# Kernel tuning notes

Hardware: AMD Instinct MI355X
Metric: run time of the kernel (lower is better)

Reference implementation:

```python
import jax, jax.numpy as jnp
import numpy as np

N = 100000   # nodes
G = 256      # graphs
E = 120000   # edges per relation
IN = 162
HID = 128
R = 5
L = 2        # extra RGCN layers beyond the initial one


def setup_inputs() -> dict:
    key = jax.random.key(0)
    ks = jax.random.split(key, 24)
    s = 0.05
    inp = {
        "X": jax.random.normal(ks[0], (N, IN), jnp.float32),
        "batch": jnp.sort(jax.random.randint(ks[6], (N,), 0, G)),
    }
    for i in range(R):
        inp[f"edge_index{i+1}"] = jax.random.randint(ks[1 + i], (2, E), 0, N)
    # RGCN initial layer params
    inp["W0"] = jax.random.normal(ks[7], (R, IN, HID), jnp.float32) * s
    inp["root0"] = jax.random.normal(ks[8], (IN, HID), jnp.float32) * s
    inp["b0"] = jnp.zeros((HID,), jnp.float32)
    # stacked params for the L hidden RGCN layers
    inp["Wl"] = jax.random.normal(ks[9], (L, R, HID, HID), jnp.float32) * s
    inp["rootl"] = jax.random.normal(ks[10], (L, HID, HID), jnp.float32) * s
    inp["bl"] = jnp.zeros((L, HID), jnp.float32)
    # classification head
    inp["Wc1"] = jax.random.normal(ks[11], (HID, HID), jnp.float32) * s
    inp["bc1"] = jnp.zeros((HID,), jnp.float32)
    inp["Wc2"] = jax.random.normal(ks[12], (HID, HID), jnp.float32) * s
    inp["bc2"] = jnp.zeros((HID,), jnp.float32)
    inp["Wc3"] = jax.random.normal(ks[13], (HID, 1), jnp.float32) * s
    inp["bc3"] = jnp.zeros((1,), jnp.float32)
    return inp


def _seg_mean(msg, dst, num):
    # scatter-mean over destination nodes (PyG RGCNConv uses aggr='mean' per relation)
    s = jax.ops.segment_sum(msg, dst, num_segments=num)
    c = jax.ops.segment_sum(jnp.ones(msg.shape[0], msg.dtype), dst, num_segments=num)
    return s / jnp.maximum(c, 1.0)[:, None]


def _rgcn(x, W, root, b, src, dst):
    # src, dst: [R, E]; W: [R, d_in, d_out]
    msgs = jnp.einsum("ref,rfh->reh", x[src], W)          # [R, E, HID]
    agg = jax.vmap(_seg_mean, in_axes=(0, 0, None))(msgs, dst, N)  # [R, N, HID]
    return x @ root + b + agg.sum(0)


def reference(X, edge_index1, edge_index2, edge_index3, edge_index4, edge_index5,
              batch, W0, root0, b0, Wl, rootl, bl, Wc1, bc1, Wc2, bc2, Wc3, bc3):
    ei = jnp.stack([edge_index1, edge_index2, edge_index3, edge_index4, edge_index5])  # [R,2,E]
    src, dst = ei[:, 0, :], ei[:, 1, :]
    h = jax.nn.relu(_rgcn(X, W0, root0, b0, src, dst))
    for l in range(L):
        h = jax.nn.relu(_rgcn(h, Wl[l], rootl[l], bl[l], src, dst))
    # mean readout over graphs
    s = jax.ops.segment_sum(h, batch, num_segments=G)
    c = jax.ops.segment_sum(jnp.ones((N,), h.dtype), batch, num_segments=G)
    read = s / jnp.maximum(c, 1.0)[:, None]
    h = jax.nn.relu(read @ Wc1 + bc1)
    h = jax.nn.relu(h @ Wc2 + bc2)
    return h @ Wc3 + bc3
```

## Files before the change

### kernel.cpp

```cpp
#include <hip/hip_runtime.h>

#define N_NODES 100000
#define NPAD    100096
#define NTILES  782
#define TPX     98
#define G_GRAPHS 256
#define IN_F 162
#define KPAD0 192
#define HID 128
#define R_REL 5
#define L_LAYERS 2
#define M5 (R_REL * N_NODES)

typedef __attribute__((ext_vector_type(8))) short bf16x8;
typedef __attribute__((ext_vector_type(4))) float f32x4;

__device__ __forceinline__ short f2bf(float f) {
    union { float f; unsigned u; } v; v.f = f;
    unsigned r = (v.u + 0x7fffu + ((v.u >> 16) & 1u)) >> 16;
    return (short)r;
}
__device__ __forceinline__ float bf2f(unsigned short u) {
    union { unsigned u; float f; } v; v.u = ((unsigned)u) << 16;
    return v.f;
}

__global__ void k_count(const int* e0, const int* e1, const int* e2,
                        const int* e3, const int* e4, int* cnt, int E) {
    int gid = blockIdx.x * 256 + threadIdx.x;
    if (gid >= R_REL * E) return;
    int r = gid / E, e = gid - r * E;
    const int* ei = (r == 0) ? e0 : (r == 1) ? e1 : (r == 2) ? e2 : (r == 3) ? e3 : e4;
    atomicAdd(&cnt[r * N_NODES + ei[E + e]], 1);
}

__global__ __launch_bounds__(256) void k_scan1(const int* __restrict__ cnt,
                                               int* __restrict__ off, int* __restrict__ bsum) {
    __shared__ int ts[256];
    int t = threadIdx.x;
    int base = blockIdx.x * 1024 + t * 4;
    int v[4];
    #pragma unroll
    for (int j = 0; j < 4; j++) {
        int d = base + j;
        int s = 0;
        if (d < N_NODES) {
            #pragma unroll
            for (int r = 0; r < R_REL; r++) s += cnt[r * N_NODES + d];
        }
        v[j] = s;
    }
    int tsum = v[0] + v[1] + v[2] + v[3];
    ts[t] = tsum; __syncthreads();
    for (int o = 1; o < 256; o <<= 1) {
        int x = (t >= o) ? ts[t - o] : 0;
        __syncthreads();
        ts[t] += x;
        __syncthreads();
    }
    if (t == 255) bsum[blockIdx.x] = ts[255];
    int run = ts[t] - tsum;
    #pragma unroll
    for (int j = 0; j < 4; j++) { if (base + j < N_NODES) off[base + j] = run; run += v[j]; }
}

__global__ __launch_bounds__(512) void k_scan2(int* bsum, int nblk) {
    __shared__ int ts[512];
    int t = threadIdx.x;
    int v = (t < nblk) ? bsum[t] : 0;
    ts[t] = v; __syncthreads();
    for (int o = 1; o < 512; o <<= 1) {
        int x = (t >= o) ? ts[t - o] : 0;
        __syncthreads();
        ts[t] += x;
        __syncthreads();
    }
    if (t < nblk) bsum[t] = ts[t] - v;
}

__global__ void k_scan3(const int* __restrict__ off, const int* __restrict__ bsum,
                        int* __restrict__ mstart, int* __restrict__ mcur,
                        const int* __restrict__ cnt, float* __restrict__ invc) {
    int i = blockIdx.x * 256 + threadIdx.x;
    if (i >= N_NODES) return;
    int o = off[i] + bsum[i >> 10];
    mstart[i] = o;
    mcur[i] = o;
    int tc = 0;
    #pragma unroll
    for (int r = 0; r < R_REL; r++) {
        int c = cnt[r * N_NODES + i];
        tc += c;
        invc[r * N_NODES + i] = 1.0f / (float)max(c, 1);
    }
    if (i == N_NODES - 1) mstart[N_NODES] = o + tc;
}

__global__ void k_fill(const int* e0, const int* e1, const int* e2,
                       const int* e3, const int* e4, int* mcur,
                       const float* __restrict__ invc,
                       int* __restrict__ mrec, float* __restrict__ mw, int E) {
    int gid = blockIdx.x * 256 + threadIdx.x;
    if (gid >= R_REL * E) return;
    int r = gid / E, e = gid - r * E;
    const int* ei = (r == 0) ? e0 : (r == 1) ? e1 : (r == 2) ? e2 : (r == 3) ? e3 : e4;
    int src = ei[e], dst = ei[E + e];
    int pos = atomicAdd(&mcur[dst], 1);
    mrec[pos] = ((1 + r) * NPAD + src) * HID;
    mw[pos] = invc[r * N_NODES + dst];
}

__global__ void k_castX(const float* __restrict__ X, unsigned short* __restrict__ Xb) {
    int gid = blockIdx.x * 256 + threadIdx.x;
    if (gid >= NPAD * KPAD0) return;
    int row = gid / KPAD0, k = gid - row * KPAD0;
    float v = (row < N_NODES && k < IN_F) ? X[(size_t)row * IN_F + k] : 0.f;
    Xb[gid] = (unsigned short)f2bf(v);
}

__global__ void k_tw0(const float* __restrict__ root0, const float* __restrict__ W0,
                      short* __restrict__ out) {
    int gid = blockIdx.x * 256 + threadIdx.x;
    if (gid >= 6 * 128 * KPAD0) return;
    int chunk = gid / (128 * KPAD0);
    int rem = gid - chunk * 128 * KPAD0;
    int col = rem / KPAD0;
    int k = rem - col * KPAD0;
    float v = 0.f;
    if (k < IN_F)
        v = (chunk == 0) ? root0[k * HID + col]
                         : W0[((size_t)(chunk - 1) * IN_F + k) * HID + col];
    out[gid] = f2bf(v);
}

__global__ void k_twl(const float* __restrict__ rootl, const float* __restrict__ Wl,
                      short* __restrict__ out) {
    int gid = blockIdx.x * 256 + threadIdx.x;
    if (gid >= L_LAYERS * 6 * 128 * HID) return;
    int l = gid / (6 * 128 * HID);
    int rem = gid - l * 6 * 128 * HID;
    int chunk = rem / (128 * HID);
    int rem2 = rem - chunk * 128 * HID;
    int col = rem2 / HID;
    int k = rem2 - col * HID;
    float v = (chunk == 0) ? rootl[((size_t)l * HID + k) * HID + col]
                           : Wl[(((size_t)l * R_REL + (chunk - 1)) * HID + k) * HID + col];
    out[gid] = f2bf(v);
}

template<int KP>
__global__ __launch_bounds__(256)
void gemm_direct(const unsigned short* __restrict__ A, const short* __restrict__ Wt,
                 unsigned short* __restrict__ Y) {
    constexpr int KS = KP / 32;
    constexpr int PF = (KS > 4) ? 2 : KS;
    constexpr int SA = KP + 8;
    __shared__ short Bs[128 * SA];

    int bid = blockIdx.x;
    int xcd = bid & 7, slot = bid >> 3;
    int chunk = slot / TPX;
    int rt = xcd * TPX + (slot - chunk * TPX);
    if (rt >= NTILES) return;
    const int row0 = rt * 128;

    const int tid = threadIdx.x;
    const int lane = tid & 63, wv = tid >> 6;
    const int quad = lane >> 4, l16 = lane & 15;
    const int wr0 = (wv >> 1) * 64, wc0 = (wv & 1) * 64;

    const size_t arow = (size_t)(row0 + wr0 + l16) * KP + quad * 8;

    bf16x8 cur[PF][4], nxt[PF][4];
    #pragma unroll
    for (int p = 0; p < PF; p++)
        #pragma unroll
        for (int i = 0; i < 4; i++)
            cur[p][i] = *(const bf16x8*)&A[arow + (size_t)i * 16 * KP + p * 32];

    const short* Wc = Wt + (size_t)chunk * 128 * KP;
    for (int cidx = tid; cidx < 128 * (KP / 8); cidx += 256) {
        int row = cidx / (KP / 8), c8 = cidx - row * (KP / 8);
        *(bf16x8*)&Bs[row * SA + c8 * 8] = *(const bf16x8*)&Wc[row * KP + c8 * 8];
    }
    __syncthreads();

    f32x4 acc[4][4];
    #pragma unroll
    for (int i = 0; i < 4; i++)
        #pragma unroll
        for (int j = 0; j < 4; j++) acc[i][j] = (f32x4){0.f, 0.f, 0.f, 0.f};

    for (int kb = 0; kb < KS; kb += PF) {
        if (kb + PF < KS) {
            #pragma unroll
            for (int p = 0; p < PF; p++)
                #pragma unroll
                for (int i = 0; i < 4; i++)
                    nxt[p][i] = *(const bf16x8*)&A[arow + (size_t)i * 16 * KP + (kb + PF + p) * 32];
        }
        #pragma unroll
        for (int p = 0; p < PF; p++) {
            int k0 = (kb + p) * 32;
            bf16x8 bfr[4];
            #pragma unroll
            for (int j = 0; j < 4; j++)
                bfr[j] = *(const bf16x8*)&Bs[(wc0 + j * 16 + l16) * SA + k0 + quad * 8];
            #pragma unroll
            for (int i = 0; i < 4; i++)
                #pragma unroll
                for (int j = 0; j < 4; j++)
                    acc[i][j] = __builtin_amdgcn_mfma_f32_16x16x32_bf16(cur[p][i], bfr[j], acc[i][j], 0, 0, 0);
        }
        #pragma unroll
        for (int p = 0; p < PF; p++)
            #pragma unroll
            for (int i = 0; i < 4; i++)
                cur[p][i] = nxt[p][i];
    }
    __syncthreads();

    #pragma unroll
    for (int i = 0; i < 4; i++)
        #pragma unroll
        for (int j = 0; j < 4; j++)
            #pragma unroll
            for (int reg = 0; reg < 4; reg++)
                Bs[(wr0 + i * 16 + quad * 4 + reg) * SA + wc0 + j * 16 + l16] =
                    f2bf(acc[i][j][reg]);
    __syncthreads();

    unsigned short* Yc = Y + (size_t)chunk * NPAD * HID + (size_t)row0 * HID;
    #pragma unroll
    for (int s = 0; s < 8; s++) {
        int row = (tid >> 4) + s * 16;
        int col = (tid & 15) * 8;
        bf16x8 v = *(const bf16x8*)&Bs[row * SA + col];
        *(bf16x8*)&Yc[(size_t)row * HID + col] = v;
    }
}

__global__ __launch_bounds__(256)
void aggregate(const unsigned short* __restrict__ Yall, const int* __restrict__ mstart,
               const int* __restrict__ mrec, const float* __restrict__ mw,
               const float* __restrict__ bias, unsigned short* __restrict__ hout) {
    int wid = (blockIdx.x * 256 + threadIdx.x) >> 6;
    int lane = threadIdx.x & 63;
    if (wid >= N_NODES) return;
    int d = wid;
    int s = mstart[d], e = mstart[d + 1];

    float2 b2 = *(const float2*)&bias[lane * 2];
    unsigned rv = *(const unsigned*)&Yall[(size_t)d * HID + lane * 2];
    float s0 = b2.x + bf2f((unsigned short)(rv & 0xffff));
    float s1 = b2.y + bf2f((unsigned short)(rv >> 16));

    for (int base = s; base < e; base += 64) {
        int m = e - base;
        int rec = 0; float w = 0.f;
        if (lane < m) { rec = mrec[base + lane]; w = mw[base + lane]; }
        int cnt = min(m, 64);
        for (int j = 0; j < cnt; j++) {
            int off = __shfl(rec, j, 64);
            float wj = __shfl(w, j, 64);
            unsigned v = *(const unsigned*)&Yall[(size_t)off + lane * 2];
            s0 += wj * bf2f((unsigned short)(v & 0xffff));
            s1 += wj * bf2f((unsigned short)(v >> 16));
        }
    }
    unsigned lo = (unsigned short)f2bf(fmaxf(s0, 0.f));
    unsigned hi = (unsigned short)f2bf(fmaxf(s1, 0.f));
    *(unsigned*)&hout[(size_t)d * HID + lane * 2] = lo | (hi << 16);
}

__global__ __launch_bounds__(128)
void k_pool(const unsigned short* __restrict__ h, const int* __restrict__ batch,
            float* __restrict__ pooled) {
    int c = threadIdx.x;
    int start = blockIdx.x * 128;
    if (start >= N_NODES) return;
    int end = min(start + 128, N_NODES);
    int g = batch[start];
    float s = 0.f;
    for (int i = start; i < end; i++) {
        int gi = batch[i];
        if (gi != g) { atomicAdd(&pooled[g * HID + c], s); s = 0.f; g = gi; }
        s += bf2f(h[(size_t)i * HID + c]);
    }
    atomicAdd(&pooled[g * HID + c], s);
}

__device__ int lower_bound_i(const int* a, int n, int v) {
    int lo = 0, hi = n;
    while (lo < hi) {
        int mid = (lo + hi) >> 1;
        if (a[mid] < v) lo = mid + 1; else hi = mid;
    }
    return lo;
}

__global__ __launch_bounds__(128)
void k_mlp(const float* __restrict__ pooled, const int* __restrict__ batch,
           const float* __restrict__ Wc1, const float* __restrict__ bc1,
           const float* __restrict__ Wc2, const float* __restrict__ bc2,
           const float* __restrict__ Wc3, const float* __restrict__ bc3,
           float* __restrict__ out) {
    int g = blockIdx.x;
    int c = threadIdx.x;
    __shared__ int range[2];
    if (c == 0) range[0] = lower_bound_i(batch, N_NODES, g);
    if (c == 1) range[1] = lower_bound_i(batch, N_NODES, g + 1);
    __syncthreads();
    float denom = fmaxf((float)(range[1] - range[0]), 1.0f);
    __shared__ float row[HID], h1[HID], h2[HID];
    row[c] = pooled[g * HID + c] / denom;
    __syncthreads();
    float acc = bc1[c];
    for (int k = 0; k < HID; k++) acc += row[k] * Wc1[k * HID + c];
    h1[c] = fmaxf(acc, 0.f);
    __syncthreads();
    acc = bc2[c];
    for (int k = 0; k < HID; k++) acc += h1[k] * Wc2[k * HID + c];
    h2[c] = fmaxf(acc, 0.f);
    __syncthreads();
    float t = h2[c] * Wc3[c];
    for (int off = 32; off > 0; off >>= 1) t += __shfl_down(t, off, 64);
    __shared__ float part[2];
    if ((c & 63) == 0) part[c >> 6] = t;
    __syncthreads();
    if (c == 0) out[g] = part[0] + part[1] + bc3[0];
}

extern "C" void kernel_launch(void* const* d_in, const int* in_sizes, int n_in,
                              void* d_out, int out_size, void* d_ws, size_t ws_size,
                              hipStream_t stream) {
    const float* X     = (const float*)d_in[0];
    const int*   batch = (const int*)d_in[1];
    const int*   e0 = (const int*)d_in[2];
    const int*   e1 = (const int*)d_in[3];
    const int*   e2 = (const int*)d_in[4];
    const int*   e3 = (const int*)d_in[5];
    const int*   e4 = (const int*)d_in[6];
    const float* W0    = (const float*)d_in[7];
    const float* root0 = (const float*)d_in[8];
    const float* b0    = (const float*)d_in[9];
    const float* Wl    = (const float*)d_in[10];
    const float* rootl = (const float*)d_in[11];
    const float* bl    = (const float*)d_in[12];
    const float* Wc1   = (const float*)d_in[13];
    const float* bc1   = (const float*)d_in[14];
    const float* Wc2   = (const float*)d_in[15];
    const float* bc2   = (const float*)d_in[16];
    const float* Wc3   = (const float*)d_in[17];
    const float* bc3   = (const float*)d_in[18];
    const int E = in_sizes[2] / 2;
    const int NE = R_REL * E;

    char* base = (char*)d_ws;
    size_t o = 0;
    auto carve = [&](size_t bytes) -> char* {
        char* p = base + o;
        o = (o + bytes + 255) & ~(size_t)255;
        return p;
    };
    unsigned short* Y    = (unsigned short*)carve((size_t)6 * NPAD * HID * 2);
    unsigned short* hA   = (unsigned short*)carve((size_t)NPAD * HID * 2);
    unsigned short* hB   = (unsigned short*)carve((size_t)NPAD * HID * 2);
    unsigned short* Xb   = (unsigned short*)carve((size_t)NPAD * KPAD0 * 2);
    int*   cnt    = (int*)carve((size_t)M5 * 4);
    float* invc   = (float*)carve((size_t)M5 * 4);
    int*   offsc  = (int*)carve((size_t)N_NODES * 4);
    int*   mstart = (int*)carve((size_t)(N_NODES + 1) * 4);
    int*   mcur   = (int*)carve((size_t)N_NODES * 4);
    int*   mrec   = (int*)carve((size_t)NE * 4);
    float* mw     = (float*)carve((size_t)NE * 4);
    int*   bsum   = (int*)carve(2048);
    float* pooled = (float*)carve((size_t)G_GRAPHS * HID * 4);
    short* Wt0    = (short*)carve((size_t)6 * 128 * KPAD0 * 2);
    short* Wtl    = (short*)carve((size_t)L_LAYERS * 6 * 128 * HID * 2);

    hipMemsetAsync(cnt, 0, (size_t)M5 * 4, stream);
    hipMemsetAsync(pooled, 0, (size_t)G_GRAPHS * HID * 4, stream);
    int eg = (NE + 255) / 256;
    k_count<<<eg, 256, 0, stream>>>(e0, e1, e2, e3, e4, cnt, E);
    int nblk = (N_NODES + 1023) / 1024;
    k_scan1<<<nblk, 256, 0, stream>>>(cnt, offsc, bsum);
    k_scan2<<<1, 512, 0, stream>>>(bsum, nblk);
    k_scan3<<<(N_NODES + 255) / 256, 256, 0, stream>>>(offsc, bsum, mstart, mcur, cnt, invc);
    k_fill<<<eg, 256, 0, stream>>>(e0, e1, e2, e3, e4, mcur, invc, mrec, mw, E);
    k_castX<<<(NPAD * KPAD0 + 255) / 256, 256, 0, stream>>>(X, Xb);
    k_tw0<<<(6 * 128 * KPAD0 + 255) / 256, 256, 0, stream>>>(root0, W0, Wt0);
    k_twl<<<(L_LAYERS * 6 * 128 * HID + 255) / 256, 256, 0, stream>>>(rootl, Wl, Wtl);

    int ggrid = 8 * TPX * 6;
    int agg_grid = (N_NODES + 3) / 4;

    gemm_direct<KPAD0><<<ggrid, 256, 0, stream>>>(Xb, Wt0, Y);
    aggregate<<<agg_grid, 256, 0, stream>>>(Y, mstart, mrec, mw, b0, hA);

    unsigned short* hin = hA; unsigned short* hout = hB;
    for (int l = 0; l < L_LAYERS; l++) {
        gemm_direct<HID><<<ggrid, 256, 0, stream>>>(hin, Wtl + (size_t)l * 6 * 128 * HID, Y);
        aggregate<<<agg_grid, 256, 0, stream>>>(Y, mstart, mrec, mw, bl + (size_t)l * HID, hout);
        unsigned short* t = hin; hin = hout; hout = t;
    }

    k_pool<<<(N_NODES + 127) / 128, 128, 0, stream>>>(hin, batch, pooled);
    k_mlp<<<G_GRAPHS, 128, 0, stream>>>(pooled, batch, Wc1, bc1, Wc2, bc2, Wc3, bc3, (float*)d_out);
}
```

Measured before the change: 693.3 us.

## Aggregate raw features per relation before a fused multi-segment GEMM

Reorders each RGCN layer to mean-aggregate input features per relation first, writing five aggregated feature buffers, and then runs one GEMM over the concatenated root and relation segments. Bias and ReLU move into that GEMM's epilogue. Edge records are packed as (src<<3)|rel and the per-edge weight array is dropped; the 1/count scaling is applied once per destination and relation. This removes the six-way per-relation output tensor and the separate weighted aggregation. In exchange, layer 0 gathers wider 192-column rows, the gather loop does masked accumulation across all five relations, the GEMM launches fewer blocks, and aggregated sums are rounded to bf16 before the matmul.

```diff
diff --git a/kernel.cpp b/kernel.cpp
--- a/kernel.cpp
+++ b/kernel.cpp
@@ -3,7 +3,6 @@
 #define N_NODES 100000
 #define NPAD    100096
 #define NTILES  782
-#define TPX     98
 #define G_GRAPHS 256
 #define IN_F 162
 #define KPAD0 192
@@ -98,16 +97,14 @@
 
 __global__ void k_fill(const int* e0, const int* e1, const int* e2,
                        const int* e3, const int* e4, int* mcur,
-                       const float* __restrict__ invc,
-                       int* __restrict__ mrec, float* __restrict__ mw, int E) {
+                       int* __restrict__ mrec, int E) {
     int gid = blockIdx.x * 256 + threadIdx.x;
     if (gid >= R_REL * E) return;
     int r = gid / E, e = gid - r * E;
     const int* ei = (r == 0) ? e0 : (r == 1) ? e1 : (r == 2) ? e2 : (r == 3) ? e3 : e4;
     int src = ei[e], dst = ei[E + e];
     int pos = atomicAdd(&mcur[dst], 1);
-    mrec[pos] = ((1 + r) * NPAD + src) * HID;
-    mw[pos] = invc[r * N_NODES + dst];
+    mrec[pos] = (src << 3) | r;
 }
 
 __global__ void k_castX(const float* __restrict__ X, unsigned short* __restrict__ Xb) {
@@ -148,129 +145,136 @@
     out[gid] = f2bf(v);
 }
 
-template<int KP>
+template<int NS, int SEG>
 __global__ __launch_bounds__(256)
-void gemm_direct(const unsigned short* __restrict__ A, const short* __restrict__ Wt,
-                 unsigned short* __restrict__ Y) {
-    constexpr int KS = KP / 32;
-    constexpr int PF = (KS > 4) ? 2 : KS;
-    constexpr int SA = KP + 8;
-    __shared__ short Bs[128 * SA];
-
-    int bid = blockIdx.x;
-    int xcd = bid & 7, slot = bid >> 3;
-    int chunk = slot / TPX;
-    int rt = xcd * TPX + (slot - chunk * TPX);
-    if (rt >= NTILES) return;
-    const int row0 = rt * 128;
-
-    const int tid = threadIdx.x;
-    const int lane = tid & 63, wv = tid >> 6;
-    const int quad = lane >> 4, l16 = lane & 15;
-    const int wr0 = (wv >> 1) * 64, wc0 = (wv & 1) * 64;
-
-    const size_t arow = (size_t)(row0 + wr0 + l16) * KP + quad * 8;
-
-    bf16x8 cur[PF][4], nxt[PF][4];
-    #pragma unroll
-    for (int p = 0; p < PF; p++)
-        #pragma unroll
-        for (int i = 0; i < 4; i++)
-            cur[p][i] = *(const bf16x8*)&A[arow + (size_t)i * 16 * KP + p * 32];
-
-    const short* Wc = Wt + (size_t)chunk * 128 * KP;
-    for (int cidx = tid; cidx < 128 * (KP / 8); cidx += 256) {
-        int row = cidx / (KP / 8), c8 = cidx - row * (KP / 8);
-        *(bf16x8*)&Bs[row * SA + c8 * 8] = *(const bf16x8*)&Wc[row * KP + c8 * 8];
-    }
-    __syncthreads();
-
-    f32x4 acc[4][4];
-    #pragma unroll
-    for (int i = 0; i < 4; i++)
-        #pragma unroll
-        for (int j = 0; j < 4; j++) acc[i][j] = (f32x4){0.f, 0.f, 0.f, 0.f};
-
-    for (int kb = 0; kb < KS; kb += PF) {
-        if (kb + PF < KS) {
-            #pragma unroll
-            for (int p = 0; p < PF; p++)
-                #pragma unroll
-                for (int i = 0; i < 4; i++)
-                    nxt[p][i] = *(const bf16x8*)&A[arow + (size_t)i * 16 * KP + (kb + PF + p) * 32];
-        }
-        #pragma unroll
-        for (int p = 0; p < PF; p++) {
-            int k0 = (kb + p) * 32;
-            bf16x8 bfr[4];
-            #pragma unroll
-            for (int j = 0; j < 4; j++)
-                bfr[j] = *(const bf16x8*)&Bs[(wc0 + j * 16 + l16) * SA + k0 + quad * 8];
-            #pragma unroll
-            for (int i = 0; i < 4; i++)
-                #pragma unroll
-                for (int j = 0; j < 4; j++)
-                    acc[i][j] = __builtin_amdgcn_mfma_f32_16x16x32_bf16(cur[p][i], bfr[j], acc[i][j], 0, 0, 0);
-        }
-        #pragma unroll
-        for (int p = 0; p < PF; p++)
-            #pragma unroll
-            for (int i = 0; i < 4; i++)
-                cur[p][i] = nxt[p][i];
-    }
-    __syncthreads();
-
-    #pragma unroll
-    for (int i = 0; i < 4; i++)
-        #pragma unroll
-        for (int j = 0; j < 4; j++)
-            #pragma unroll
-            for (int reg = 0; reg < 4; reg++)
-                Bs[(wr0 + i * 16 + quad * 4 + reg) * SA + wc0 + j * 16 + l16] =
-                    f2bf(acc[i][j][reg]);
-    __syncthreads();
-
-    unsigned short* Yc = Y + (size_t)chunk * NPAD * HID + (size_t)row0 * HID;
-    #pragma unroll
-    for (int s = 0; s < 8; s++) {
-        int row = (tid >> 4) + s * 16;
-        int col = (tid & 15) * 8;
-        bf16x8 v = *(const bf16x8*)&Bs[row * SA + col];
-        *(bf16x8*)&Yc[(size_t)row * HID + col] = v;
-    }
-}
-
-__global__ __launch_bounds__(256)
-void aggregate(const unsigned short* __restrict__ Yall, const int* __restrict__ mstart,
-               const int* __restrict__ mrec, const float* __restrict__ mw,
-               const float* __restrict__ bias, unsigned short* __restrict__ hout) {
+void aggregate_pre(const unsigned short* __restrict__ Xin, const int* __restrict__ mstart,
+                   const int* __restrict__ mrec, const float* __restrict__ invc,
+                   unsigned short* __restrict__ Xagg) {
     int wid = (blockIdx.x * 256 + threadIdx.x) >> 6;
     int lane = threadIdx.x & 63;
     if (wid >= N_NODES) return;
     int d = wid;
     int s = mstart[d], e = mstart[d + 1];
 
-    float2 b2 = *(const float2*)&bias[lane * 2];
-    unsigned rv = *(const unsigned*)&Yall[(size_t)d * HID + lane * 2];
-    float s0 = b2.x + bf2f((unsigned short)(rv & 0xffff));
-    float s1 = b2.y + bf2f((unsigned short)(rv >> 16));
+    float a0[R_REL], a1[R_REL], a2[R_REL];
+    #pragma unroll
+    for (int r = 0; r < R_REL; r++) { a0[r] = 0.f; a1[r] = 0.f; a2[r] = 0.f; }
 
     for (int base = s; base < e; base += 64) {
         int m = e - base;
-        int rec = 0; float w = 0.f;
-        if (lane < m) { rec = mrec[base + lane]; w = mw[base + lane]; }
+        int rec = 0;
+        if (lane < m) rec = mrec[base + lane];
         int cnt = min(m, 64);
         for (int j = 0; j < cnt; j++) {
-            int off = __shfl(rec, j, 64);
-            float wj = __shfl(w, j, 64);
-            unsigned v = *(const unsigned*)&Yall[(size_t)off + lane * 2];
-            s0 += wj * bf2f((unsigned short)(v & 0xffff));
-            s1 += wj * bf2f((unsigned short)(v >> 16));
+            int rv = __shfl(rec, j, 64);
+            int src = rv >> 3, r = rv & 7;
+            const unsigned short* row = Xin + (size_t)src * SEG;
+            unsigned u = *(const unsigned*)&row[2 * lane];
+            float v0 = bf2f((unsigned short)(u & 0xffff));
+            float v1 = bf2f((unsigned short)(u >> 16));
+            float v2 = (NS == 3) ? bf2f(row[128 + lane]) : 0.f;
+            #pragma unroll
+            for (int rr = 0; rr < R_REL; rr++) {
+                float msk = (rr == r) ? 1.f : 0.f;
+                a0[rr] += msk * v0;
+                a1[rr] += msk * v1;
+                if (NS == 3) a2[rr] += msk * v2;
+            }
         }
     }
-    unsigned lo = (unsigned short)f2bf(fmaxf(s0, 0.f));
-    unsigned hi = (unsigned short)f2bf(fmaxf(s1, 0.f));
-    *(unsigned*)&hout[(size_t)d * HID + lane * 2] = lo | (hi << 16);
+    #pragma unroll
+    for (int r = 0; r < R_REL; r++) {
+        float w = invc[r * N_NODES + d];
+        unsigned lo = (unsigned short)f2bf(a0[r] * w);
+        unsigned hi = (unsigned short)f2bf(a1[r] * w);
+        unsigned short* orow = Xagg + ((size_t)r * NPAD + d) * SEG;
+        *(unsigned*)&orow[2 * lane] = lo | (hi << 16);
+        if (NS == 3) orow[128 + lane] = (unsigned short)f2bf(a2[r] * w);
+    }
+}
+
+template<int SEG>
+__global__ __launch_bounds__(256)
+void gemm_fat(const unsigned short* __restrict__ X0,
+              const unsigned short* __restrict__ Xagg,
+              const short* __restrict__ Wt,
+              const float* __restrict__ bias,
+              unsigned short* __restrict__ H) {
+    constexpr int KSEG = SEG / 32;
+    constexpr int SA = SEG + 8;
+    __shared__ short Bs[128 * SA];
+    const int tid = threadIdx.x;
+    const int row0 = blockIdx.x * 128;
+    const int lane = tid & 63, wv = tid >> 6;
+    const int quad = lane >> 4, l16 = lane & 15;
+    const int wr0 = (wv >> 1) * 64, wc0 = (wv & 1) * 64;
+
+    float bv[4];
+    #pragma unroll
+    for (int j = 0; j < 4; j++) bv[j] = bias[wc0 + j * 16 + l16];
+
+    f32x4 acc[4][4];
+    #pragma unroll
+    for (int i = 0; i < 4; i++)
+        #pragma unroll
+        for (int j = 0; j < 4; j++) acc[i][j] = (f32x4){0.f, 0.f, 0.f, 0.f};
+
+    const int arow = row0 + wr0 + l16;
+
+    for (int seg = 0; seg < 6; seg++) {
+        const unsigned short* Ap = (seg == 0) ? X0 : Xagg + (size_t)(seg - 1) * NPAD * SEG;
+        bf16x8 cur[4], nxt[4];
+        #pragma unroll
+        for (int i = 0; i < 4; i++)
+            cur[i] = *(const bf16x8*)&Ap[(size_t)(arow + i * 16) * SEG + quad * 8];
+
+        __syncthreads();
+        const short* Wc = Wt + (size_t)seg * 128 * SEG;
+        for (int cidx = tid; cidx < 128 * (SEG / 8); cidx += 256) {
+            int r = cidx / (SEG / 8), c8 = cidx - r * (SEG / 8);
+            *(bf16x8*)&Bs[r * SA + c8 * 8] = *(const bf16x8*)&Wc[r * SEG + c8 * 8];
+        }
+        __syncthreads();
+
+        for (int kb = 0; kb < KSEG; kb++) {
+            if (kb + 1 < KSEG) {
+                #pragma unroll
+                for (int i = 0; i < 4; i++)
+                    nxt[i] = *(const bf16x8*)&Ap[(size_t)(arow + i * 16) * SEG + (kb + 1) * 32 + quad * 8];
+            }
+            bf16x8 bfr[4];
+            #pragma unroll
+            for (int j = 0; j < 4; j++)
+                bfr[j] = *(const bf16x8*)&Bs[(wc0 + j * 16 + l16) * SA + kb * 32 + quad * 8];
+            #pragma unroll
+            for (int i = 0; i < 4; i++)
+                #pragma unroll
+                for (int j = 0; j < 4; j++)
+                    acc[i][j] = __builtin_amdgcn_mfma_f32_16x16x32_bf16(cur[i], bfr[j], acc[i][j], 0, 0, 0);
+            #pragma unroll
+            for (int i = 0; i < 4; i++) cur[i] = nxt[i];
+        }
+    }
+    __syncthreads();
+
+    #pragma unroll
+    for (int i = 0; i < 4; i++)
+        #pragma unroll
+        for (int j = 0; j < 4; j++)
+            #pragma unroll
+            for (int reg = 0; reg < 4; reg++) {
+                float v = fmaxf(acc[i][j][reg] + bv[j], 0.f);
+                Bs[(wr0 + i * 16 + quad * 4 + reg) * SA + wc0 + j * 16 + l16] = f2bf(v);
+            }
+    __syncthreads();
+
+    #pragma unroll
+    for (int s = 0; s < 8; s++) {
+        int row = (tid >> 4) + s * 16;
+        int col = (tid & 15) * 8;
+        bf16x8 v = *(const bf16x8*)&Bs[row * SA + col];
+        *(bf16x8*)&H[(size_t)(row0 + row) * HID + col] = v;
+    }
 }
 
 __global__ __launch_bounds__(128)
@@ -363,9 +367,9 @@
         o = (o + bytes + 255) & ~(size_t)255;
         return p;
     };
-    unsigned short* Y    = (unsigned short*)carve((size_t)6 * NPAD * HID * 2);
+    unsigned short* xagg = (unsigned short*)carve((size_t)R_REL * NPAD * KPAD0 * 2);
+    unsigned short* hB   = xagg + (size_t)R_REL * NPAD * HID;
     unsigned short* hA   = (unsigned short*)carve((size_t)NPAD * HID * 2);
-    unsigned short* hB   = (unsigned short*)carve((size_t)NPAD * HID * 2);
     unsigned short* Xb   = (unsigned short*)carve((size_t)NPAD * KPAD0 * 2);
     int*   cnt    = (int*)carve((size_t)M5 * 4);
     float* invc   = (float*)carve((size_t)M5 * 4);
@@ -373,7 +377,6 @@
     int*   mstart = (int*)carve((size_t)(N_NODES + 1) * 4);
     int*   mcur   = (int*)carve((size_t)N_NODES * 4);
     int*   mrec   = (int*)carve((size_t)NE * 4);
-    float* mw     = (float*)carve((size_t)NE * 4);
     int*   bsum   = (int*)carve(2048);
     float* pooled = (float*)carve((size_t)G_GRAPHS * HID * 4);
     short* Wt0    = (short*)carve((size_t)6 * 128 * KPAD0 * 2);
@@ -387,24 +390,23 @@
     k_scan1<<<nblk, 256, 0, stream>>>(cnt, offsc, bsum);
     k_scan2<<<1, 512, 0, stream>>>(bsum, nblk);
     k_scan3<<<(N_NODES + 255) / 256, 256, 0, stream>>>(offsc, bsum, mstart, mcur, cnt, invc);
-    k_fill<<<eg, 256, 0, stream>>>(e0, e1, e2, e3, e4, mcur, invc, mrec, mw, E);
+    k_fill<<<eg, 256, 0, stream>>>(e0, e1, e2, e3, e4, mcur, mrec, E);
     k_castX<<<(NPAD * KPAD0 + 255) / 256, 256, 0, stream>>>(X, Xb);
     k_tw0<<<(6 * 128 * KPAD0 + 255) / 256, 256, 0, stream>>>(root0, W0, Wt0);
     k_twl<<<(L_LAYERS * 6 * 128 * HID + 255) / 256, 256, 0, stream>>>(rootl, Wl, Wtl);
 
-    int ggrid = 8 * TPX * 6;
     int agg_grid = (N_NODES + 3) / 4;
 
-    gemm_direct<KPAD0><<<ggrid, 256, 0, stream>>>(Xb, Wt0, Y);
-    aggregate<<<agg_grid, 256, 0, stream>>>(Y, mstart, mrec, mw, b0, hA);
-
-    unsigned short* hin = hA; unsigned short* hout = hB;
-    for (int l = 0; l < L_LAYERS; l++) {
-        gemm_direct<HID><<<ggrid, 256, 0, stream>>>(hin, Wtl + (size_t)l * 6 * 128 * HID, Y);
-        aggregate<<<agg_grid, 256, 0, stream>>>(Y, mstart, mrec, mw, bl + (size_t)l * HID, hout);
-        unsigned short* t = hin; hin = hout; hout = t;
-    }
-
-    k_pool<<<(N_NODES + 127) / 128, 128, 0, stream>>>(hin, batch, pooled);
+    aggregate_pre<3, KPAD0><<<agg_grid, 256, 0, stream>>>(Xb, mstart, mrec, invc, xagg);
+    gemm_fat<KPAD0><<<NTILES, 256, 0, stream>>>(Xb, xagg, Wt0, b0, hA);
+
+    aggregate_pre<2, HID><<<agg_grid, 256, 0, stream>>>(hA, mstart, mrec, invc, xagg);
+    gemm_fat<HID><<<NTILES, 256, 0, stream>>>(hA, xagg, Wtl, bl, hB);
+
+    aggregate_pre<2, HID><<<agg_grid, 256, 0, stream>>>(hB, mstart, mrec, invc, xagg);
+    gemm_fat<HID><<<NTILES, 256, 0, stream>>>(hB, xagg, Wtl + (size_t)6 * 128 * HID,
+                                              bl + HID, hA);
+
+    k_pool<<<(N_NODES + 127) / 128, 128, 0, stream>>>(hA, batch, pooled);
     k_mlp<<<G_GRAPHS, 128, 0, stream>>>(pooled, batch, Wc1, bc1, Wc2, bc2, Wc3, bc3, (float*)d_out);
 }
```

Measured after the change: 725.5 us. 1.05x slower.
